# Performance work log

Hardware: AMD Instinct MI355X
Metric: run time of the kernel (lower is better)

## Reference

```python
import jax, jax.numpy as jnp
import numpy as np

B, IN, H, M = 16384, 512, 512, 4096


def setup_inputs() -> dict:
    key = jax.random.key(0)
    ks = jax.random.split(key, 8)
    s_in = 1.0 / np.sqrt(IN + H)
    return {
        "input_tensor": jax.random.normal(ks[0], (B, IN), jnp.float32),
        "hidden": jax.random.normal(ks[1], (B, H), jnp.float32),
        "cell": jax.random.normal(ks[2], (B, H), jnp.float32),
        # fused gate weights: columns = [input, forget, cell, output] gates
        "W_gates": jax.random.normal(ks[3], (IN + H, 4 * H), jnp.float32) * s_in,
        "b_gates": jnp.zeros((4 * H,), jnp.float32),
        "W_attn": jax.random.normal(ks[4], (H, M), jnp.float32) / np.sqrt(H),
        "b_attn": jnp.zeros((M,), jnp.float32),
        "memory_matrix": jax.random.normal(ks[5], (M, H), jnp.float32) * np.sqrt(2.0 / (M + H)),
    }


def reference(input_tensor, hidden, cell, W_gates, b_gates, W_attn, b_attn, memory_matrix):
    combined = jnp.concatenate([input_tensor, hidden], axis=1)        # (B, IN+H)
    gates = combined @ W_gates + b_gates                              # (B, 4H)
    i_g, f_g, c_g, o_g = jnp.split(gates, 4, axis=1)
    i_g = jax.nn.sigmoid(i_g)
    f_g = jax.nn.sigmoid(f_g)
    c_g = jnp.tanh(c_g)
    o_g = jax.nn.sigmoid(o_g)
    attn = jax.nn.softmax(hidden @ W_attn + b_attn, axis=1)           # (B, M)
    memory_read = attn @ memory_matrix                                # (B, H)
    new_cell = f_g * cell + i_g * c_g + 0.1 * memory_read
    new_hidden = o_g * jnp.tanh(new_cell)
    return (new_hidden, new_cell, attn)
```

## Files before the change

### kernel.cpp

```cpp
#include <hip/hip_runtime.h>
#include <hip/hip_bf16.h>
#include <math.h>

typedef __bf16 bf16_t;
typedef bf16_t bf16x8 __attribute__((ext_vector_type(8)));
typedef float  f32x4  __attribute__((ext_vector_type(4)));

static constexpr int Bn = 16384;
static constexpr int Hn = 512;

__device__ __forceinline__ float sigm(float x) { return 1.0f / (1.0f + __expf(-x)); }

typedef __attribute__((address_space(3))) void lds_void;
typedef const __attribute__((address_space(1))) void gl_void;

__device__ __forceinline__ void glds16(const void* g, void* l) {
    __builtin_amdgcn_global_load_lds((gl_void*)g, (lds_void*)l, 16, 0, 0);
}

__global__ void convert_comb(const float* __restrict__ inp, const float* __restrict__ hid,
                             bf16_t* __restrict__ comb)
{
    size_t t = (size_t)blockIdx.x * blockDim.x + threadIdx.x;
    size_t r = t >> 7;
    int c8 = (int)(t & 127);
    const float* src = (c8 < 64) ? (inp + r * 512 + c8 * 8) : (hid + r * 512 + (c8 - 64) * 8);
    float4 a = ((const float4*)src)[0];
    float4 b = ((const float4*)src)[1];
    bf16x8 o;
    o[0] = (bf16_t)a.x; o[1] = (bf16_t)a.y; o[2] = (bf16_t)a.z; o[3] = (bf16_t)a.w;
    o[4] = (bf16_t)b.x; o[5] = (bf16_t)b.y; o[6] = (bf16_t)b.z; o[7] = (bf16_t)b.w;
    *(bf16x8*)(comb + t * 8) = o;
}

__global__ void transpose_all(const float* __restrict__ Wg, bf16_t* __restrict__ WgT,
                              const float* __restrict__ Wa, bf16_t* __restrict__ WaT,
                              const float* __restrict__ Mem, bf16_t* __restrict__ MemT)
{
    __shared__ float tile[32][33];
    int b = blockIdx.x;
    const float* src; bf16_t* dst; int R, C, gx;
    if (b < 2048)      { src = Wg;  dst = WgT;  R = 1024; C = 2048; gx = 64; }
    else if (b < 4096) { b -= 2048; src = Wa;  dst = WaT;  R = 512;  C = 4096; gx = 128; }
    else               { b -= 4096; src = Mem; dst = MemT; R = 4096; C = 512;  gx = 16; }
    const int x0 = (b % gx) * 32, y0 = (b / gx) * 32;
    const int tx = threadIdx.x & 31, ty = threadIdx.x >> 5;
#pragma unroll
    for (int i = 0; i < 32; i += 8)
        tile[ty + i][tx] = src[(size_t)(y0 + ty + i) * C + x0 + tx];
    __syncthreads();
#pragma unroll
    for (int i = 0; i < 32; i += 8)
        dst[(size_t)(x0 + ty + i) * R + y0 + tx] = (bf16_t)tile[tx][ty + i];
}

template<int EPI>
__global__ __launch_bounds__(512)
void gemm_w8(const bf16_t* __restrict__ A, int lda,
             const bf16_t* __restrict__ Bt, int ldb,
             const float* __restrict__ bias, int K, int N,
             bf16_t* __restrict__ bout, int ost)
{
    __shared__ __align__(16) bf16_t sA[128 * 64];
    __shared__ __align__(16) bf16_t sB[256 * 64];

    const int tid = threadIdx.x, lane = tid & 63, wid = tid >> 6;
    const int wr = wid >> 2, wc = wid & 3;

    const int nwg = gridDim.x;
    int bid = (blockIdx.x & 7) * (nwg >> 3) + (blockIdx.x >> 3);
    const int cbn = N >> 8;
    const int row0 = (bid / cbn) * 128, col0 = (bid % cbn) * 256;

    f32x4 acc[4][4] = {};
    const int nk = K >> 6;
    const int l15 = lane & 15, kq = lane >> 4;

    for (int kt = 0; kt < nk; ++kt) {
        const int k0 = kt << 6;
        {
            const int slot = (lane & 7) ^ (lane >> 3);
#pragma unroll
            for (int t = 0; t < 2; ++t) {
                const int c8 = wid * 2 + t;
                const int r = c8 * 8 + (lane >> 3);
                glds16(A + (size_t)(row0 + r) * lda + k0 + slot * 8, sA + c8 * 512);
            }
#pragma unroll
            for (int t = 0; t < 4; ++t) {
                const int c8 = wid * 4 + t;
                const int r = c8 * 8 + (lane >> 3);
                glds16(Bt + (size_t)(col0 + r) * ldb + k0 + slot * 8, sB + c8 * 512);
            }
        }
        __syncthreads();
#pragma unroll
        for (int ks = 0; ks < 2; ++ks) {
            bf16x8 af[4], bfr[4];
            const int slot = (ks * 4 + kq) ^ (l15 & 7);
#pragma unroll
            for (int j = 0; j < 4; ++j) {
                const int rb = wc * 64 + j * 16 + l15;
                bfr[j] = *(const bf16x8*)&sB[rb * 64 + slot * 8];
                const int ra = wr * 64 + j * 16 + l15;
                af[j] = *(const bf16x8*)&sA[ra * 64 + slot * 8];
            }
#pragma unroll
            for (int i = 0; i < 4; ++i)
#pragma unroll
                for (int j = 0; j < 4; ++j)
                    acc[i][j] = __builtin_amdgcn_mfma_f32_16x16x32_bf16(af[i], bfr[j], acc[i][j], 0, 0, 0);
        }
        __syncthreads();
    }

    const int lr = (lane >> 4) * 4, lc = lane & 15;
#pragma unroll
    for (int i = 0; i < 4; ++i) {
#pragma unroll
        for (int j = 0; j < 4; ++j) {
#pragma unroll
            for (int r = 0; r < 4; ++r) {
                const int grow = row0 + wr * 64 + i * 16 + lr + r;
                const int gcol = col0 + wc * 64 + j * 16 + lc;
                float v = acc[i][j][r] + bias[gcol];
                if constexpr (EPI == 0) {
                    const float a = ((gcol >> 9) == 2) ? tanhf(v) : sigm(v);
                    bout[(size_t)grow * 2048 + gcol] = (bf16_t)a;
                } else {
                    bout[(size_t)grow * ost + gcol] = (bf16_t)v;
                }
            }
        }
    }
}

__global__ __launch_bounds__(512)
void gemm3k(const bf16_t* __restrict__ Ap, int astride,
            const bf16_t* __restrict__ MemT,
            const bf16_t* __restrict__ gates, const float* __restrict__ cell,
            float* __restrict__ fout)
{
    __shared__ __align__(16) bf16_t sA[64 * 64];
    __shared__ __align__(16) bf16_t sB[256 * 64];

    const int tid = threadIdx.x, lane = tid & 63, wid = tid >> 6;
    const int wr = wid >> 2, wc = wid & 3;

    int bid = (blockIdx.x & 7) * 64 + (blockIdx.x >> 3);
    const int row0 = (bid >> 1) * 64, col0 = (bid & 1) * 256;

    f32x4 acc[2][4] = {};
    const int l15 = lane & 15, kq = lane >> 4;

    for (int kt = 0; kt < 64; ++kt) {
        const int k0 = kt << 6;
        const int slot = (lane & 7) ^ (lane >> 3);
        {
            const int c8 = wid;
            const int r = c8 * 8 + (lane >> 3);
            glds16(Ap + (size_t)(row0 + r) * astride + k0 + slot * 8, sA + c8 * 512);
        }
#pragma unroll
        for (int t = 0; t < 4; ++t) {
            const int c8 = wid * 4 + t;
            const int r = c8 * 8 + (lane >> 3);
            glds16(MemT + (size_t)(col0 + r) * 4096 + k0 + slot * 8, sB + c8 * 512);
        }
        __syncthreads();
#pragma unroll
        for (int ks = 0; ks < 2; ++ks) {
            bf16x8 af[2], bfr[4];
            const int sl = (ks * 4 + kq) ^ (l15 & 7);
#pragma unroll
            for (int j = 0; j < 4; ++j) {
                const int rb = wc * 64 + j * 16 + l15;
                bfr[j] = *(const bf16x8*)&sB[rb * 64 + sl * 8];
            }
#pragma unroll
            for (int i = 0; i < 2; ++i) {
                const int ra = wr * 32 + i * 16 + l15;
                af[i] = *(const bf16x8*)&sA[ra * 64 + sl * 8];
            }
#pragma unroll
            for (int i = 0; i < 2; ++i)
#pragma unroll
                for (int j = 0; j < 4; ++j)
                    acc[i][j] = __builtin_amdgcn_mfma_f32_16x16x32_bf16(af[i], bfr[j], acc[i][j], 0, 0, 0);
        }
        __syncthreads();
    }

    const int lr = (lane >> 4) * 4, lc = lane & 15;
#pragma unroll
    for (int i = 0; i < 2; ++i) {
#pragma unroll
        for (int j = 0; j < 4; ++j) {
#pragma unroll
            for (int r = 0; r < 4; ++r) {
                const int grow = row0 + wr * 32 + i * 16 + lr + r;
                const int gcol = col0 + wc * 64 + j * 16 + lc;
                const float v = acc[i][j][r];
                const float ig = (float)gates[(size_t)grow * 2048 + gcol];
                const float fg = (float)gates[(size_t)grow * 2048 + 512 + gcol];
                const float cg = (float)gates[(size_t)grow * 2048 + 1024 + gcol];
                const float og = (float)gates[(size_t)grow * 2048 + 1536 + gcol];
                const float cv = cell[(size_t)grow * 512 + gcol];
                const float ncv = fg * cv + ig * cg + 0.1f * v;
                fout[(size_t)grow * 512 + gcol] = og * tanhf(ncv);
                fout[(size_t)Bn * Hn + (size_t)grow * 512 + gcol] = ncv;
            }
        }
    }
}

template<bool F32OUT>
__global__ void softmax_k(bf16_t* __restrict__ packed, int pstride, float* __restrict__ attnf32)
{
    const int row = blockIdx.x;
    bf16_t* lp = packed + (size_t)row * pstride;
    const int tid = threadIdx.x;

    float v[16];
    {
        bf16x8 h0 = ((const bf16x8*)lp)[tid];
        bf16x8 h1 = ((const bf16x8*)lp)[tid + 256];
#pragma unroll
        for (int k = 0; k < 8; ++k) { v[k] = (float)h0[k]; v[8 + k] = (float)h1[k]; }
    }
    float mx = v[0];
#pragma unroll
    for (int k = 1; k < 16; ++k) mx = fmaxf(mx, v[k]);
#pragma unroll
    for (int off = 32; off > 0; off >>= 1) mx = fmaxf(mx, __shfl_xor(mx, off));
    __shared__ float smx[4], ssm[4];
    if ((tid & 63) == 0) smx[tid >> 6] = mx;
    __syncthreads();
    mx = fmaxf(fmaxf(smx[0], smx[1]), fmaxf(smx[2], smx[3]));

    float sum = 0.0f;
#pragma unroll
    for (int k = 0; k < 16; ++k) { v[k] = __expf(v[k] - mx); sum += v[k]; }
#pragma unroll
    for (int off = 32; off > 0; off >>= 1) sum += __shfl_xor(sum, off);
    if ((tid & 63) == 0) ssm[tid >> 6] = sum;
    __syncthreads();
    sum = ssm[0] + ssm[1] + ssm[2] + ssm[3];

    const float inv = 1.0f / sum;
#pragma unroll
    for (int k = 0; k < 16; ++k) v[k] *= inv;

    bf16x8 o0, o1;
#pragma unroll
    for (int k = 0; k < 8; ++k) { o0[k] = (bf16_t)v[k]; o1[k] = (bf16_t)v[8 + k]; }
    ((bf16x8*)lp)[tid]       = o0;
    ((bf16x8*)lp)[tid + 256] = o1;

    if constexpr (F32OUT) {
        float* rp = attnf32 + (size_t)row * 4096;
        float4 a0 = { v[0], v[1], v[2], v[3] },   a1 = { v[4], v[5], v[6], v[7] };
        float4 a2 = { v[8], v[9], v[10], v[11] }, a3 = { v[12], v[13], v[14], v[15] };
        ((float4*)rp)[2 * tid]             = a0;
        ((float4*)rp)[2 * tid + 1]         = a1;
        ((float4*)rp)[2 * (tid + 256)]     = a2;
        ((float4*)rp)[2 * (tid + 256) + 1] = a3;
    }
}

__global__ void expand_attn(float* __restrict__ attn)
{
    const int row = blockIdx.x;
    float* rp = attn + (size_t)row * 4096;
    const int t = threadIdx.x;
    bf16x8 h0 = ((const bf16x8*)rp)[2 * t];
    bf16x8 h1 = ((const bf16x8*)rp)[2 * t + 1];
    __syncthreads();
    float4 o0 = { (float)h0[0], (float)h0[1], (float)h0[2], (float)h0[3] };
    float4 o1 = { (float)h0[4], (float)h0[5], (float)h0[6], (float)h0[7] };
    float4 o2 = { (float)h1[0], (float)h1[1], (float)h1[2], (float)h1[3] };
    float4 o3 = { (float)h1[4], (float)h1[5], (float)h1[6], (float)h1[7] };
    ((float4*)rp)[4 * t]     = o0;
    ((float4*)rp)[4 * t + 1] = o1;
    ((float4*)rp)[4 * t + 2] = o2;
    ((float4*)rp)[4 * t + 3] = o3;
}

extern "C" void kernel_launch(void* const* d_in, const int* in_sizes, int n_in,
                              void* d_out, int out_size, void* d_ws, size_t ws_size,
                              hipStream_t stream)
{
    const float* input  = (const float*)d_in[0];
    const float* hidden = (const float*)d_in[1];
    const float* cell   = (const float*)d_in[2];
    const float* Wg     = (const float*)d_in[3];
    const float* bg     = (const float*)d_in[4];
    const float* Wa     = (const float*)d_in[5];
    const float* ba     = (const float*)d_in[6];
    const float* Mem    = (const float*)d_in[7];

    float* out  = (float*)d_out;
    float* attn = out + 2ull * Bn * Hn;

    bf16_t* comb  = (bf16_t*)d_ws;
    bf16_t* WgT   = comb + (size_t)Bn * 1024;
    bf16_t* WaT   = WgT + (size_t)2048 * 1024;
    bf16_t* MemT  = WaT + (size_t)4096 * 512;
    bf16_t* gates = MemT + (size_t)512 * 4096;
    bf16_t* pws   = gates + (size_t)Bn * 2048;

    const size_t need_big = ((size_t)Bn * 1024 + 2048 * 1024 + 4096 * 512 + 512 * 4096
                             + (size_t)Bn * 2048 + (size_t)Bn * 4096) * sizeof(bf16_t);
    const bool big = ws_size >= need_big;
    bf16_t* packed = big ? pws : (bf16_t*)attn;
    const int pstride = big ? 4096 : 8192;

    convert_comb<<<8192, 256, 0, stream>>>(input, hidden, comb);
    transpose_all<<<6144, 256, 0, stream>>>(Wg, WgT, Wa, WaT, Mem, MemT);

    gemm_w8<0><<<1024, 512, 0, stream>>>(comb, 1024, WgT, 1024, bg, 1024, 2048, gates, 2048);
    gemm_w8<1><<<2048, 512, 0, stream>>>(comb + 512, 1024, WaT, 512, ba, 512, 4096,
                                         packed, pstride);

    if (big) softmax_k<true><<<Bn, 256, 0, stream>>>(packed, pstride, attn);
    else     softmax_k<false><<<Bn, 256, 0, stream>>>(packed, pstride, nullptr);

    gemm3k<<<512, 512, 0, stream>>>(packed, pstride, MemT, gates, cell, out);

    if (!big) expand_attn<<<Bn, 256, 0, stream>>>(attn);
}
```

Measured before the change: 462.0 us.

## Double-buffer LDS tiles in both GEMM kernels to overlap loads with MFMA

Both GEMM kernels now keep two LDS buffers for A and B tiles. The next k-tile is issued with global_load_lds before the current one is computed, and partial vmcnt waits plus raw barriers replace the full syncthreads. This is meant to hide global-load latency behind MFMA work, at the cost of doubled LDS use (up to 96KB in gemm_w8), which may lower occupancy.

```diff
diff --git a/kernel.cpp b/kernel.cpp
--- a/kernel.cpp
+++ b/kernel.cpp
@@ -61,8 +61,8 @@
              const float* __restrict__ bias, int K, int N,
              bf16_t* __restrict__ bout, int ost)
 {
-    __shared__ __align__(16) bf16_t sA[128 * 64];
-    __shared__ __align__(16) bf16_t sB[256 * 64];
+    __shared__ __align__(16) bf16_t sA[2][128 * 64];
+    __shared__ __align__(16) bf16_t sB[2][256 * 64];
 
     const int tid = threadIdx.x, lane = tid & 63, wid = tid >> 6;
     const int wr = wid >> 2, wc = wid & 3;
@@ -75,25 +75,25 @@
     f32x4 acc[4][4] = {};
     const int nk = K >> 6;
     const int l15 = lane & 15, kq = lane >> 4;
-
-    for (int kt = 0; kt < nk; ++kt) {
+    const int sslot = (lane & 7) ^ (lane >> 3);
+
+    auto stage = [&](int b, int kt) {
         const int k0 = kt << 6;
-        {
-            const int slot = (lane & 7) ^ (lane >> 3);
-#pragma unroll
-            for (int t = 0; t < 2; ++t) {
-                const int c8 = wid * 2 + t;
-                const int r = c8 * 8 + (lane >> 3);
-                glds16(A + (size_t)(row0 + r) * lda + k0 + slot * 8, sA + c8 * 512);
-            }
-#pragma unroll
-            for (int t = 0; t < 4; ++t) {
-                const int c8 = wid * 4 + t;
-                const int r = c8 * 8 + (lane >> 3);
-                glds16(Bt + (size_t)(col0 + r) * ldb + k0 + slot * 8, sB + c8 * 512);
-            }
-        }
-        __syncthreads();
+#pragma unroll
+        for (int t = 0; t < 2; ++t) {
+            const int c8 = wid * 2 + t;
+            const int r = c8 * 8 + (lane >> 3);
+            glds16(A + (size_t)(row0 + r) * lda + k0 + sslot * 8, &sA[b][c8 * 512]);
+        }
+#pragma unroll
+        for (int t = 0; t < 4; ++t) {
+            const int c8 = wid * 4 + t;
+            const int r = c8 * 8 + (lane >> 3);
+            glds16(Bt + (size_t)(col0 + r) * ldb + k0 + sslot * 8, &sB[b][c8 * 512]);
+        }
+    };
+
+    auto compute = [&](int b) {
 #pragma unroll
         for (int ks = 0; ks < 2; ++ks) {
             bf16x8 af[4], bfr[4];
@@ -101,9 +101,9 @@
 #pragma unroll
             for (int j = 0; j < 4; ++j) {
                 const int rb = wc * 64 + j * 16 + l15;
-                bfr[j] = *(const bf16x8*)&sB[rb * 64 + slot * 8];
+                bfr[j] = *(const bf16x8*)&sB[b][rb * 64 + slot * 8];
                 const int ra = wr * 64 + j * 16 + l15;
-                af[j] = *(const bf16x8*)&sA[ra * 64 + slot * 8];
+                af[j] = *(const bf16x8*)&sA[b][ra * 64 + slot * 8];
             }
 #pragma unroll
             for (int i = 0; i < 4; ++i)
@@ -111,8 +111,22 @@
                 for (int j = 0; j < 4; ++j)
                     acc[i][j] = __builtin_amdgcn_mfma_f32_16x16x32_bf16(af[i], bfr[j], acc[i][j], 0, 0, 0);
         }
-        __syncthreads();
-    }
+    };
+
+    stage(0, 0);
+    for (int kt = 0; kt < nk - 1; ++kt) {
+        stage((kt + 1) & 1, kt + 1);
+        asm volatile("s_waitcnt vmcnt(6)" ::: "memory");
+        __builtin_amdgcn_sched_barrier(0);
+        __builtin_amdgcn_s_barrier();
+        compute(kt & 1);
+        __builtin_amdgcn_sched_barrier(0);
+        __builtin_amdgcn_s_barrier();
+    }
+    asm volatile("s_waitcnt vmcnt(0)" ::: "memory");
+    __builtin_amdgcn_sched_barrier(0);
+    __builtin_amdgcn_s_barrier();
+    compute((nk - 1) & 1);
 
     const int lr = (lane >> 4) * 4, lc = lane & 15;
 #pragma unroll
@@ -141,8 +155,8 @@
             const bf16_t* __restrict__ gates, const float* __restrict__ cell,
             float* __restrict__ fout)
 {
-    __shared__ __align__(16) bf16_t sA[64 * 64];
-    __shared__ __align__(16) bf16_t sB[256 * 64];
+    __shared__ __align__(16) bf16_t sA[2][64 * 64];
+    __shared__ __align__(16) bf16_t sB[2][256 * 64];
 
     const int tid = threadIdx.x, lane = tid & 63, wid = tid >> 6;
     const int wr = wid >> 2, wc = wid & 3;
@@ -152,22 +166,24 @@
 
     f32x4 acc[2][4] = {};
     const int l15 = lane & 15, kq = lane >> 4;
-
-    for (int kt = 0; kt < 64; ++kt) {
+    const int sslot = (lane & 7) ^ (lane >> 3);
+
+    auto stage = [&](int b, int kt) {
         const int k0 = kt << 6;
-        const int slot = (lane & 7) ^ (lane >> 3);
         {
             const int c8 = wid;
             const int r = c8 * 8 + (lane >> 3);
-            glds16(Ap + (size_t)(row0 + r) * astride + k0 + slot * 8, sA + c8 * 512);
+            glds16(Ap + (size_t)(row0 + r) * astride + k0 + sslot * 8, &sA[b][c8 * 512]);
         }
 #pragma unroll
         for (int t = 0; t < 4; ++t) {
             const int c8 = wid * 4 + t;
             const int r = c8 * 8 + (lane >> 3);
-            glds16(MemT + (size_t)(col0 + r) * 4096 + k0 + slot * 8, sB + c8 * 512);
-        }
-        __syncthreads();
+            glds16(MemT + (size_t)(col0 + r) * 4096 + k0 + sslot * 8, &sB[b][c8 * 512]);
+        }
+    };
+
+    auto compute = [&](int b) {
 #pragma unroll
         for (int ks = 0; ks < 2; ++ks) {
             bf16x8 af[2], bfr[4];
@@ -175,12 +191,12 @@
 #pragma unroll
             for (int j = 0; j < 4; ++j) {
                 const int rb = wc * 64 + j * 16 + l15;
-                bfr[j] = *(const bf16x8*)&sB[rb * 64 + sl * 8];
+                bfr[j] = *(const bf16x8*)&sB[b][rb * 64 + sl * 8];
             }
 #pragma unroll
             for (int i = 0; i < 2; ++i) {
                 const int ra = wr * 32 + i * 16 + l15;
-                af[i] = *(const bf16x8*)&sA[ra * 64 + sl * 8];
+                af[i] = *(const bf16x8*)&sA[b][ra * 64 + sl * 8];
             }
 #pragma unroll
             for (int i = 0; i < 2; ++i)
@@ -188,8 +204,22 @@
                 for (int j = 0; j < 4; ++j)
                     acc[i][j] = __builtin_amdgcn_mfma_f32_16x16x32_bf16(af[i], bfr[j], acc[i][j], 0, 0, 0);
         }
-        __syncthreads();
-    }
+    };
+
+    stage(0, 0);
+    for (int kt = 0; kt < 63; ++kt) {
+        stage((kt + 1) & 1, kt + 1);
+        asm volatile("s_waitcnt vmcnt(5)" ::: "memory");
+        __builtin_amdgcn_sched_barrier(0);
+        __builtin_amdgcn_s_barrier();
+        compute(kt & 1);
+        __builtin_amdgcn_sched_barrier(0);
+        __builtin_amdgcn_s_barrier();
+    }
+    asm volatile("s_waitcnt vmcnt(0)" ::: "memory");
+    __builtin_amdgcn_sched_barrier(0);
+    __builtin_amdgcn_s_barrier();
+    compute(1);
 
     const int lr = (lane >> 4) * 4, lc = lane & 15;
 #pragma unroll
```

Result: slower. 514.9 us (+11.5%).

## Double-buffer LDS and enlarge tiles to 256x256 in gate/attention GEMMs

Applied to the files above, without the earlier changes.

The gemm_w8 kernel now uses 256x256 output tiles (8x4 accumulators per wave) instead of 128x256, and double-buffers the A/B LDS tiles so the next K-slice's global->LDS loads are issued before computing the current one. Explicit vmcnt waits and raw s_barriers replace __syncthreads. Grid sizes are halved to match. The aim is to raise arithmetic intensity and overlap loads with MFMA work, at the cost of much more LDS (128 KB) and more accumulator registers, which may limit occupancy.

```diff
diff --git a/kernel.cpp b/kernel.cpp
--- a/kernel.cpp
+++ b/kernel.cpp
@@ -55,14 +55,14 @@
 }
 
 template<int EPI>
-__global__ __launch_bounds__(512)
+__global__ __launch_bounds__(512, 2)
 void gemm_w8(const bf16_t* __restrict__ A, int lda,
              const bf16_t* __restrict__ Bt, int ldb,
              const float* __restrict__ bias, int K, int N,
              bf16_t* __restrict__ bout, int ost)
 {
-    __shared__ __align__(16) bf16_t sA[128 * 64];
-    __shared__ __align__(16) bf16_t sB[256 * 64];
+    __shared__ __align__(16) bf16_t sA[2][256 * 64];
+    __shared__ __align__(16) bf16_t sB[2][256 * 64];
 
     const int tid = threadIdx.x, lane = tid & 63, wid = tid >> 6;
     const int wr = wid >> 2, wc = wid & 3;
@@ -70,58 +70,75 @@
     const int nwg = gridDim.x;
     int bid = (blockIdx.x & 7) * (nwg >> 3) + (blockIdx.x >> 3);
     const int cbn = N >> 8;
-    const int row0 = (bid / cbn) * 128, col0 = (bid % cbn) * 256;
-
-    f32x4 acc[4][4] = {};
+    const int row0 = (bid / cbn) * 256, col0 = (bid % cbn) * 256;
+
+    f32x4 acc[8][4] = {};
     const int nk = K >> 6;
     const int l15 = lane & 15, kq = lane >> 4;
-
-    for (int kt = 0; kt < nk; ++kt) {
+    const int sslot = (lane & 7) ^ (lane >> 3);
+
+    auto stage = [&](int b, int kt) {
         const int k0 = kt << 6;
-        {
-            const int slot = (lane & 7) ^ (lane >> 3);
-#pragma unroll
-            for (int t = 0; t < 2; ++t) {
-                const int c8 = wid * 2 + t;
-                const int r = c8 * 8 + (lane >> 3);
-                glds16(A + (size_t)(row0 + r) * lda + k0 + slot * 8, sA + c8 * 512);
-            }
-#pragma unroll
-            for (int t = 0; t < 4; ++t) {
-                const int c8 = wid * 4 + t;
-                const int r = c8 * 8 + (lane >> 3);
-                glds16(Bt + (size_t)(col0 + r) * ldb + k0 + slot * 8, sB + c8 * 512);
-            }
-        }
-        __syncthreads();
+#pragma unroll
+        for (int t = 0; t < 4; ++t) {
+            const int c8 = wid * 4 + t;
+            const int r = c8 * 8 + (lane >> 3);
+            glds16(A + (size_t)(row0 + r) * lda + k0 + sslot * 8, &sA[b][c8 * 512]);
+            glds16(Bt + (size_t)(col0 + r) * ldb + k0 + sslot * 8, &sB[b][c8 * 512]);
+        }
+    };
+
+    auto compute = [&](int b) {
 #pragma unroll
         for (int ks = 0; ks < 2; ++ks) {
-            bf16x8 af[4], bfr[4];
             const int slot = (ks * 4 + kq) ^ (l15 & 7);
+            bf16x8 bfr[4];
 #pragma unroll
             for (int j = 0; j < 4; ++j) {
                 const int rb = wc * 64 + j * 16 + l15;
-                bfr[j] = *(const bf16x8*)&sB[rb * 64 + slot * 8];
-                const int ra = wr * 64 + j * 16 + l15;
-                af[j] = *(const bf16x8*)&sA[ra * 64 + slot * 8];
-            }
-#pragma unroll
-            for (int i = 0; i < 4; ++i)
-#pragma unroll
-                for (int j = 0; j < 4; ++j)
-                    acc[i][j] = __builtin_amdgcn_mfma_f32_16x16x32_bf16(af[i], bfr[j], acc[i][j], 0, 0, 0);
-        }
-        __syncthreads();
+                bfr[j] = *(const bf16x8*)&sB[b][rb * 64 + slot * 8];
+            }
+#pragma unroll
+            for (int ih = 0; ih < 2; ++ih) {
+                bf16x8 af[4];
+#pragma unroll
+                for (int i = 0; i < 4; ++i) {
+                    const int ra = wr * 128 + (ih * 4 + i) * 16 + l15;
+                    af[i] = *(const bf16x8*)&sA[b][ra * 64 + slot * 8];
+                }
+#pragma unroll
+                for (int i = 0; i < 4; ++i)
+#pragma unroll
+                    for (int j = 0; j < 4; ++j)
+                        acc[ih * 4 + i][j] = __builtin_amdgcn_mfma_f32_16x16x32_bf16(
+                            af[i], bfr[j], acc[ih * 4 + i][j], 0, 0, 0);
+            }
+        }
+    };
+
+    stage(0, 0);
+    for (int kt = 0; kt < nk; ++kt) {
+        if (kt + 1 < nk) {
+            stage((kt + 1) & 1, kt + 1);
+            asm volatile("s_waitcnt vmcnt(8)" ::: "memory");
+        } else {
+            asm volatile("s_waitcnt vmcnt(0)" ::: "memory");
+        }
+        __builtin_amdgcn_sched_barrier(0);
+        __builtin_amdgcn_s_barrier();
+        compute(kt & 1);
+        __builtin_amdgcn_sched_barrier(0);
+        __builtin_amdgcn_s_barrier();
     }
 
     const int lr = (lane >> 4) * 4, lc = lane & 15;
 #pragma unroll
-    for (int i = 0; i < 4; ++i) {
+    for (int i = 0; i < 8; ++i) {
 #pragma unroll
         for (int j = 0; j < 4; ++j) {
 #pragma unroll
             for (int r = 0; r < 4; ++r) {
-                const int grow = row0 + wr * 64 + i * 16 + lr + r;
+                const int grow = row0 + wr * 128 + i * 16 + lr + r;
                 const int gcol = col0 + wc * 64 + j * 16 + lc;
                 float v = acc[i][j][r] + bias[gcol];
                 if constexpr (EPI == 0) {
@@ -318,8 +335,8 @@
     convert_comb<<<8192, 256, 0, stream>>>(input, hidden, comb);
     transpose_all<<<6144, 256, 0, stream>>>(Wg, WgT, Wa, WaT, Mem, MemT);
 
-    gemm_w8<0><<<1024, 512, 0, stream>>>(comb, 1024, WgT, 1024, bg, 1024, 2048, gates, 2048);
-    gemm_w8<1><<<2048, 512, 0, stream>>>(comb + 512, 1024, WaT, 512, ba, 512, 4096,
+    gemm_w8<0><<<512, 512, 0, stream>>>(comb, 1024, WgT, 1024, bg, 1024, 2048, gates, 2048);
+    gemm_w8<1><<<1024, 512, 0, stream>>>(comb + 512, 1024, WaT, 512, ba, 512, 4096,
                                          packed, pstride);
 
     if (big) softmax_k<true><<<Bn, 256, 0, stream>>>(packed, pstride, attn);
```

Result: slower. 492.6 us (+6.6%).

## Rewrite gate and attention GEMMs as double-buffered 256x256 pipelined kernel

Applied to the files above, without the earlier changes.

Replaces the 128x256 single-buffered GEMM with a 256x256 tile kernel that double-buffers K-slices in 128KB of dynamic LDS. Global-to-LDS loads for upcoming stages are interleaved with MFMA phases, using explicit vmcnt waits, barriers and setprio. The aim is to hide global load latency behind compute and to raise operand reuse per tile. In exchange each workgroup holds more accumulator registers and uses large LDS, which lowers occupancy. The hand-written wait counts must also line up exactly with the staging order, or the results will be wrong.

```diff
diff --git a/kernel.cpp b/kernel.cpp
--- a/kernel.cpp
+++ b/kernel.cpp
@@ -54,74 +54,126 @@
         dst[(size_t)(x0 + ty + i) * R + y0 + tx] = (bf16_t)tile[tx][ty + i];
 }
 
+#define VM4 do { asm volatile("s_waitcnt vmcnt(4)" ::: "memory"); \
+                 __builtin_amdgcn_sched_barrier(0); } while (0)
+#define VM0 do { asm volatile("s_waitcnt vmcnt(0)" ::: "memory"); \
+                 __builtin_amdgcn_sched_barrier(0); } while (0)
+#define NOP ((void)0)
+
+#define PH(d, ks, hi, READB, STAGE, WAIT) do {                                     \
+    bf16x8 af_[4];                                                                 \
+    _Pragma("unroll")                                                              \
+    for (int ii = 0; ii < 4; ++ii)                                                 \
+        af_[ii] = *(const bf16x8*)&lds[(d)*16384 + (ks)*8192 +                     \
+                                       ((hi)*64 + ii*16)*64 + abr];                \
+    if (READB) {                                                                   \
+        _Pragma("unroll")                                                          \
+        for (int j = 0; j < 4; ++j)                                                \
+            bfr[j] = *(const bf16x8*)&lds[32768 + (d)*16384 + (ks)*8192 +          \
+                                          j*1024 + bbr];                           \
+    }                                                                              \
+    STAGE;                                                                         \
+    WAIT;                                                                          \
+    __builtin_amdgcn_s_barrier();                                                  \
+    __builtin_amdgcn_s_setprio(1);                                                 \
+    _Pragma("unroll")                                                              \
+    for (int ii = 0; ii < 4; ++ii)                                                 \
+        _Pragma("unroll")                                                          \
+        for (int j = 0; j < 4; ++j)                                                \
+            acc[(hi)*4 + ii][j] = __builtin_amdgcn_mfma_f32_16x16x32_bf16(         \
+                af_[ii], bfr[j], acc[(hi)*4 + ii][j], 0, 0, 0);                    \
+    __builtin_amdgcn_s_setprio(0);                                                 \
+    __builtin_amdgcn_s_barrier();                                                  \
+    __builtin_amdgcn_sched_barrier(0);                                             \
+} while (0)
+
 template<int EPI>
-__global__ __launch_bounds__(512)
-void gemm_w8(const bf16_t* __restrict__ A, int lda,
-             const bf16_t* __restrict__ Bt, int ldb,
-             const float* __restrict__ bias, int K, int N,
-             bf16_t* __restrict__ bout, int ost)
-{
-    __shared__ __align__(16) bf16_t sA[128 * 64];
-    __shared__ __align__(16) bf16_t sB[256 * 64];
+__global__ __launch_bounds__(512, 2)
+void gemm8p(const bf16_t* __restrict__ A, int lda,
+            const bf16_t* __restrict__ Bt, int ldb,
+            const float* __restrict__ bias, int K, int N,
+            bf16_t* __restrict__ bout, int ost)
+{
+    extern __shared__ __align__(16) bf16_t lds[];
 
     const int tid = threadIdx.x, lane = tid & 63, wid = tid >> 6;
     const int wr = wid >> 2, wc = wid & 3;
+    const int l15 = lane & 15, kq = lane >> 4;
 
     const int nwg = gridDim.x;
     int bid = (blockIdx.x & 7) * (nwg >> 3) + (blockIdx.x >> 3);
     const int cbn = N >> 8;
-    const int row0 = (bid / cbn) * 128, col0 = (bid % cbn) * 256;
-
-    f32x4 acc[4][4] = {};
-    const int nk = K >> 6;
-    const int l15 = lane & 15, kq = lane >> 4;
-
-    for (int kt = 0; kt < nk; ++kt) {
-        const int k0 = kt << 6;
-        {
-            const int slot = (lane & 7) ^ (lane >> 3);
-#pragma unroll
-            for (int t = 0; t < 2; ++t) {
-                const int c8 = wid * 2 + t;
-                const int r = c8 * 8 + (lane >> 3);
-                glds16(A + (size_t)(row0 + r) * lda + k0 + slot * 8, sA + c8 * 512);
-            }
-#pragma unroll
-            for (int t = 0; t < 4; ++t) {
-                const int c8 = wid * 4 + t;
-                const int r = c8 * 8 + (lane >> 3);
-                glds16(Bt + (size_t)(col0 + r) * ldb + k0 + slot * 8, sB + c8 * 512);
-            }
-        }
-        __syncthreads();
-#pragma unroll
-        for (int ks = 0; ks < 2; ++ks) {
-            bf16x8 af[4], bfr[4];
-            const int slot = (ks * 4 + kq) ^ (l15 & 7);
-#pragma unroll
-            for (int j = 0; j < 4; ++j) {
-                const int rb = wc * 64 + j * 16 + l15;
-                bfr[j] = *(const bf16x8*)&sB[rb * 64 + slot * 8];
-                const int ra = wr * 64 + j * 16 + l15;
-                af[j] = *(const bf16x8*)&sA[ra * 64 + slot * 8];
-            }
-#pragma unroll
-            for (int i = 0; i < 4; ++i)
-#pragma unroll
-                for (int j = 0; j < 4; ++j)
-                    acc[i][j] = __builtin_amdgcn_mfma_f32_16x16x32_bf16(af[i], bfr[j], acc[i][j], 0, 0, 0);
-        }
-        __syncthreads();
+    const int row0 = (bid / cbn) * 256, col0 = (bid % cbn) * 256;
+
+    const int sl  = (lane & 7) ^ (lane >> 3);
+    const int smh = sl >> 2, sq = sl & 3;
+    size_t goffA[2], goffB[2];
+    int ldsoff[2];
+#pragma unroll
+    for (int t = 0; t < 2; ++t) {
+        const int c8 = wid * 2 + t;
+        const int prow = c8 * 8 + (lane >> 3);
+        goffA[t] = (size_t)(row0 + smh * 128 + prow) * lda + sq * 8;
+        goffB[t] = (size_t)(col0 + smh * 128 + prow) * ldb + sq * 8;
+        ldsoff[t] = c8 * 512;
+    }
+
+    const int abr = l15 * 64 + (((wr * 4 + kq) ^ (l15 & 7)) * 8);
+    const int bbr = ((wc & 1) * 64 + l15) * 64 + ((((wc >> 1) * 4 + kq) ^ (l15 & 7)) * 8);
+
+    auto stageA = [&](int d, int kh, int kt) {
+        const int koff = kt * 64 + kh * 32;
+#pragma unroll
+        for (int t = 0; t < 2; ++t)
+            glds16(A + goffA[t] + koff, lds + d * 16384 + kh * 8192 + ldsoff[t]);
+    };
+    auto stageB = [&](int d, int kh, int kt) {
+        const int koff = kt * 64 + kh * 32;
+#pragma unroll
+        for (int t = 0; t < 2; ++t)
+            glds16(Bt + goffB[t] + koff, lds + 32768 + d * 16384 + kh * 8192 + ldsoff[t]);
+    };
+
+    f32x4 acc[8][4] = {};
+    bf16x8 bfr[4];
+
+    stageA(0, 0, 0); stageB(0, 0, 0); stageA(0, 1, 0); stageB(0, 1, 0);
+    stageA(1, 0, 1); stageB(1, 0, 1);
+    VM4;
+    __builtin_amdgcn_s_barrier();
+
+    const int niter = K >> 7;
+    for (int it = 0; it < niter - 1; ++it) {
+        const int o = 2 * it + 1, e2 = 2 * it + 2, o2 = 2 * it + 3;
+        PH(0, 0, 0, 1, stageA(1, 1, o),  NOP);
+        PH(0, 0, 1, 0, stageB(1, 1, o),  NOP);
+        PH(0, 1, 0, 1, stageA(0, 0, e2), NOP);
+        PH(0, 1, 1, 0, stageB(0, 0, e2), VM4);
+        PH(1, 0, 0, 1, stageA(0, 1, e2), NOP);
+        PH(1, 0, 1, 0, stageB(0, 1, e2), NOP);
+        PH(1, 1, 0, 1, stageA(1, 0, o2), NOP);
+        PH(1, 1, 1, 0, stageB(1, 0, o2), VM4);
+    }
+    {
+        const int o = 2 * niter - 1;
+        PH(0, 0, 0, 1, stageA(1, 1, o), NOP);
+        PH(0, 0, 1, 0, stageB(1, 1, o), NOP);
+        PH(0, 1, 0, 1, NOP, NOP);
+        PH(0, 1, 1, 0, NOP, VM0);
+        PH(1, 0, 0, 1, NOP, NOP);
+        PH(1, 0, 1, 0, NOP, NOP);
+        PH(1, 1, 0, 1, NOP, NOP);
+        PH(1, 1, 1, 0, NOP, NOP);
     }
 
     const int lr = (lane >> 4) * 4, lc = lane & 15;
 #pragma unroll
-    for (int i = 0; i < 4; ++i) {
+    for (int i = 0; i < 8; ++i) {
 #pragma unroll
         for (int j = 0; j < 4; ++j) {
 #pragma unroll
             for (int r = 0; r < 4; ++r) {
-                const int grow = row0 + wr * 64 + i * 16 + lr + r;
+                const int grow = row0 + wr * 128 + i * 16 + lr + r;
                 const int gcol = col0 + wc * 64 + j * 16 + lc;
                 float v = acc[i][j][r] + bias[gcol];
                 if constexpr (EPI == 0) {
@@ -315,12 +367,18 @@
     bf16_t* packed = big ? pws : (bf16_t*)attn;
     const int pstride = big ? 4096 : 8192;
 
+    hipFuncSetAttribute((const void*)gemm8p<0>,
+                        hipFuncAttributeMaxDynamicSharedMemorySize, 131072);
+    hipFuncSetAttribute((const void*)gemm8p<1>,
+                        hipFuncAttributeMaxDynamicSharedMemorySize, 131072);
+
     convert_comb<<<8192, 256, 0, stream>>>(input, hidden, comb);
     transpose_all<<<6144, 256, 0, stream>>>(Wg, WgT, Wa, WaT, Mem, MemT);
 
-    gemm_w8<0><<<1024, 512, 0, stream>>>(comb, 1024, WgT, 1024, bg, 1024, 2048, gates, 2048);
-    gemm_w8<1><<<2048, 512, 0, stream>>>(comb + 512, 1024, WaT, 512, ba, 512, 4096,
-                                         packed, pstride);
+    gemm8p<0><<<512, 512, 131072, stream>>>(comb, 1024, WgT, 1024, bg, 1024, 2048,
+                                            gates, 2048);
+    gemm8p<1><<<1024, 512, 131072, stream>>>(comb + 512, 1024, WaT, 512, ba, 512, 4096,
+                                             packed, pstride);
 
     if (big) softmax_k<true><<<Bn, 256, 0, stream>>>(packed, pstride, attn);
     else     softmax_k<false><<<Bn, 256, 0, stream>>>(packed, pstride, nullptr);
```

New measurement: 490.9 us. 1.06x slower.
